# Kernel optimization log

Hardware: AMD Instinct MI355X
Metric: run time of the kernel (lower is better)

Reference implementation:

```python
import jax, jax.numpy as jnp
import numpy as np

BATCH = 4096
INPUT = 14271   # genes
HIDDEN = 24     # gene sets
NUM_ENRICH = 2
EPS = 1e-5          # BatchNorm1d default eps
MAXRANK_PARAM = 1000.0

@jax.custom_vjp
def ste(x):
    # straight-through binarization: forward (x > 0), backward hardtanh(grad)
    return (x > 0).astype(x.dtype)

def _ste_fwd(x):
    return ste(x), None

def _ste_bwd(res, g):
    return (jnp.clip(g, -1.0, 1.0),)

ste.defvjp(_ste_fwd, _ste_bwd)

def setup_inputs() -> dict:
    key = jax.random.key(0)
    ks = jax.random.split(key, 7)
    # ranks in [0, 20000) so that the maxrank clamp is actually exercised
    x_rank = jax.random.uniform(ks[0], (BATCH, INPUT), dtype=jnp.float32) * 20000.0
    x_log2 = jax.random.uniform(ks[1], (BATCH, INPUT), dtype=jnp.float32) * 10.0
    B = jax.random.uniform(ks[2], (INPUT, INPUT), dtype=jnp.float32)
    # matches torch init: normal(mean=-0.1, std=0.055)
    weight = jax.random.normal(ks[3], (INPUT, HIDDEN), dtype=jnp.float32) * 0.055 - 0.1
    maxrank_p = jax.random.uniform(ks[4], (1, 1), dtype=jnp.float32)
    out_w = jax.random.normal(ks[5], (1, HIDDEN * NUM_ENRICH), dtype=jnp.float32) * 0.05
    out_b = jnp.zeros((1,), dtype=jnp.float32)
    return {"x_rank": x_rank, "x_log2": x_log2, "B": B,
            "weight": weight, "maxrank_p": maxrank_p,
            "out_w": out_w, "out_b": out_b}

def reference(x_rank, x_log2, B, weight, maxrank_p, out_w, out_b):
    W = ste(weight)                         # [G, H] binary {0,1}
    n = W.sum(0)[None, :]                   # [1, H] genes per set
    maxrank = n.max() + 10.0 + jnp.maximum(maxrank_p, 0.0) * MAXRANK_PARAM  # [1,1]
    xr = jnp.minimum(x_rank, maxrank)       # clamp ranks
    R = xr @ W                              # [B, H]
    R_UCell = 1.0 - (R - n * (n + 1.0) / 2.0) / (n * maxrank)
    gs_backgrounds = B @ W                  # [G, H]
    bg_score = (x_log2 @ gs_backgrounds) / gs_backgrounds.sum(0)  # [B, H]
    raw_score = (x_log2 @ W) / W.sum(0)     # [B, H]
    R_AMS = raw_score - bg_score
    R_all = jnp.concatenate([R_UCell, R_AMS], axis=1)   # [B, 2H]
    # BatchNorm1d(affine=False), training-mode batch statistics (biased var)
    mu = R_all.mean(0)
    var = R_all.var(0)
    R_norm = (R_all - mu) * jax.lax.rsqrt(var + EPS)
    # dropout treated as identity (eval mode) for deterministic reference
    pred = R_norm @ out_w.T + out_b         # [B, 1]
    return pred
```

## Files before the change

kernel.cpp:

```cpp
#include <hip/hip_runtime.h>
#include <hip/hip_bf16.h>

#define BATCH 4096
#define G     14271
#define H     24
#define KT    446
#define NIT   223
#define MB1   223
#define MBX   64
#define S1    8
#define SX    16
#define IPS1  28
#define IPSX  14
#define GP    14272
#define LDSTR 68
#define FMAX  3.402823466e38f

typedef __bf16 bf16x8 __attribute__((ext_vector_type(8)));
typedef float  f32x4  __attribute__((ext_vector_type(4)));

__device__ inline unsigned short bf16_bits(float f) {
    __bf16 h = (__bf16)f;
    return __builtin_bit_cast(unsigned short, h);
}
__device__ inline float bits_to_f32(unsigned short b) {
    return __builtin_bit_cast(float, (unsigned int)b << 16);
}


__global__ void k_counts(const float* __restrict__ w, int* __restrict__ counts) {
    int g = blockIdx.x * blockDim.x + threadIdx.x;
    bool valid = g < G;
    const float* row = w + (long)g * H;
#pragma unroll
    for (int h = 0; h < H; ++h) {
        bool bit = valid && (row[h] > 0.0f);
        unsigned long long ball = __ballot(bit);
        if ((threadIdx.x & 63) == 0) atomicAdd(&counts[h], (int)__popcll(ball));
    }
}

__global__ void k_consts(const int* __restrict__ counts,
                         const float* __restrict__ maxrank_p,
                         float* __restrict__ consts) {
    __shared__ float smr;
    int t = threadIdx.x;
    if (t == 0) {
        int nm = 0;
        for (int h = 0; h < H; ++h) nm = max(nm, counts[h]);
        float mp = maxrank_p[0];
        if (mp < 0.0f) mp = 0.0f;
        smr = (float)nm + 10.0f + mp * 1000.0f;
        consts[24] = smr;
    }
    __syncthreads();
    if (t < H) {
        float n  = (float)counts[t];
        float mr = smr;
        float c1 = n * (n + 1.0f) * 0.5f;
        float c2 = 1.0f / (n * mr);
        consts[t]      = n;
        consts[32 + t] = 1.0f + c1 * c2;
        consts[56 + t] = c2;
        consts[80 + t] = 1.0f / n;
    }
}

__global__ void k_fillfrag(const float* __restrict__ w,
                           unsigned short* __restrict__ W01f,
                           unsigned short* __restrict__ C2f) {
    int id = blockIdx.x * blockDim.x + threadIdx.x;
    const int nW = KT * 2 * 64;
    const int nC = KT * 3 * 64;
    unsigned short* dst;
    int NT, tl;
    if (id < nW)       { dst = W01f; NT = 2; tl = id; }
    else               { tl = id - nW; if (tl >= nC) return; dst = C2f; NT = 3; }
    int lane  = tl & 63;
    int tile  = tl >> 6;
    int ktile = tile / NT;
    int nt    = tile % NT;
    int col   = nt * 16 + (lane & 15);
    int kbase = ktile * 32 + (lane >> 4) * 8;
    if (dst == C2f && col >= 24) return;
    unsigned short v[8];
#pragma unroll
    for (int j = 0; j < 8; ++j) {
        int k = kbase + j;
        v[j] = (k < G && col < H && (w[(long)k * H + col] > 0.0f))
                   ? (unsigned short)0x3F80 : (unsigned short)0;
    }
    unsigned short* p = dst + ((long)tile * 64 + lane) * 8;
#pragma unroll
    for (int j = 0; j < 8; ++j) p[j] = v[j];
}


__device__ inline void stage_tile(const float* __restrict__ A, int M, int row0,
                                  int k0, bool clampk, float* buf,
                                  int wave, int lane) {
    int k = k0 + lane;
    if (clampk) k = (k < G) ? k : (G - 1);
#pragma unroll
    for (int i = 0; i < 16; ++i) {
        int r = wave * 16 + i;
        int grow = row0 + r;
        grow = (grow < M) ? grow : (M - 1);
        const float* src = A + (long)grow * G + k;
        __builtin_amdgcn_global_load_lds(
            (const __attribute__((address_space(1))) void*)src,
            (__attribute__((address_space(3))) void*)(buf + r * LDSTR),
            4, 0, 0);
    }
}

template <int NT>
__device__ inline void consume_tiles(const float* __restrict__ buf,
                                     const unsigned short* __restrict__ Wf,
                                     int ktile0, float mr, f32x4* acc,
                                     int wave, int lane) {
    int r = lane & 15, sub = lane >> 4;
    const float* rowp = buf + (wave * 16 + r) * LDSTR + sub * 8;
#pragma unroll
    for (int kt = 0; kt < 2; ++kt) {
        const float4* p = reinterpret_cast<const float4*>(rowp + kt * 32);
        float4 lo = p[0];
        float4 hi = p[1];
        float a[8] = {lo.x, lo.y, lo.z, lo.w, hi.x, hi.y, hi.z, hi.w};
        bf16x8 af;
#pragma unroll
        for (int j = 0; j < 8; ++j) af[j] = (__bf16)fminf(a[j], mr);
        const unsigned short* fb = Wf + ((long)((ktile0 + kt) * NT) * 64 + lane) * 8;
#pragma unroll
        for (int nt = 0; nt < NT; ++nt) {
            bf16x8 bfr = *reinterpret_cast<const bf16x8*>(fb + (long)nt * 512);
            acc[nt] = __builtin_amdgcn_mfma_f32_16x16x32_bf16(af, bfr, acc[nt], 0, 0, 0);
        }
    }
}

template <int NT>
__device__ inline void gemm_block(const float* __restrict__ A, int M, int mblk,
                                  const unsigned short* __restrict__ Wf, float mr,
                                  int it0, int it1,
                                  float* __restrict__ outp, int ldo) {
    __shared__ __align__(16) float sbuf[2][64 * LDSTR];
    int wave = threadIdx.x >> 6, lane = threadIdx.x & 63;
    int row0 = mblk * 64;
    f32x4 acc[NT];
#pragma unroll
    for (int nt = 0; nt < NT; ++nt) acc[nt] = (f32x4){0.f, 0.f, 0.f, 0.f};

    stage_tile(A, M, row0, it0 * 64, it0 == NIT - 1, sbuf[0], wave, lane);
    __syncthreads();
    int cur = 0;
    for (int it = it0; it < it1; ++it) {
        if (it + 1 < it1)
            stage_tile(A, M, row0, (it + 1) * 64, (it + 1) == NIT - 1,
                       sbuf[cur ^ 1], wave, lane);
        consume_tiles<NT>(sbuf[cur], Wf, it * 2, mr, acc, wave, lane);
        __syncthreads();
        cur ^= 1;
    }
    int ocol  = lane & 15;
    int sub   = lane >> 4;
    int orow0 = row0 + wave * 16 + sub * 4;
#pragma unroll
    for (int nt = 0; nt < NT; ++nt)
#pragma unroll
        for (int rr = 0; rr < 4; ++rr) {
            int orow = orow0 + rr;
            if (orow < M) outp[(long)orow * ldo + nt * 16 + ocol] = acc[nt][rr];
        }
}

__global__ __launch_bounds__(256) void k_gemm2(
    const float* __restrict__ Bmat, const float* __restrict__ xrank,
    const unsigned short* __restrict__ W01f, const float* __restrict__ consts,
    float* __restrict__ p1, float* __restrict__ rp) {
    int bid = blockIdx.x;
    if (bid < MB1 * S1) {
        int mblk = bid >> 3, split = bid & 7;
        int it0 = split * IPS1;
        int it1 = min(it0 + IPS1, NIT);
        gemm_block<2>(Bmat, G, mblk, W01f, FMAX, it0, it1,
                      p1 + (long)split * GP * 32, 32);
    } else {
        int t = bid - MB1 * S1;
        int mblk = t >> 4, split = t & 15;
        int it0 = split * IPSX;
        int it1 = min(it0 + IPSX, NIT);
        gemm_block<2>(xrank, BATCH, mblk, W01f, consts[24], it0, it1,
                      rp + (long)split * BATCH * 32, 32);
    }
}

__global__ __launch_bounds__(256) void k_gemm3(
    const float* __restrict__ xlog2, const unsigned short* __restrict__ C2f,
    float* __restrict__ lp) {
    int bid = blockIdx.x;
    int mblk = bid >> 4, split = bid & 15;
    int it0 = split * IPSX;
    int it1 = min(it0 + IPSX, NIT);
    gemm_block<3>(xlog2, BATCH, mblk, C2f, FMAX, it0, it1,
                  lp + (long)split * BATCH * 48, 48);
}

__global__ __launch_bounds__(256) void k_reduce1(const float* __restrict__ p1,
                                                 unsigned short* __restrict__ C2f,
                                                 float* __restrict__ blockS) {
    int k = blockIdx.x * 256 + threadIdx.x;
    float gsr[H];
#pragma unroll
    for (int h = 0; h < H; ++h) gsr[h] = 0.0f;
    if (k < GP) {
        if (k < G) {
            for (int sp = 0; sp < S1; ++sp) {
                const float4* r4 = reinterpret_cast<const float4*>(
                    p1 + ((long)sp * GP + k) * 32);
#pragma unroll
                for (int q = 0; q < 6; ++q) {
                    float4 v = r4[q];
                    gsr[q * 4 + 0] += v.x;
                    gsr[q * 4 + 1] += v.y;
                    gsr[q * 4 + 2] += v.z;
                    gsr[q * 4 + 3] += v.w;
                }
            }
        }
        int ktile = k >> 5, j = k & 7, lsub = (k >> 3) & 3;
#pragma unroll
        for (int h = 0; h < H; ++h) {
            unsigned short bits = bf16_bits(gsr[h]);
            int col = 24 + h, nt = col >> 4, lane = lsub * 16 + (col & 15);
            C2f[((long)(ktile * 3 + nt) * 64 + lane) * 8 + j] = bits;
            gsr[h] = bits_to_f32(bits);
        }
    }
    __shared__ float sred[4][H];
    int lane = threadIdx.x & 63, w = threadIdx.x >> 6;
#pragma unroll
    for (int h = 0; h < H; ++h) {
        float v = gsr[h];
        for (int off = 1; off < 64; off <<= 1) v += __shfl_xor(v, off);
        if (lane == 0) sred[w][h] = v;
    }
    __syncthreads();
    if (threadIdx.x < H) {
        float s = sred[0][threadIdx.x] + sred[1][threadIdx.x] +
                  sred[2][threadIdx.x] + sred[3][threadIdx.x];
        blockS[blockIdx.x * H + threadIdx.x] = s;
    }
}

__global__ void k_sumS(const float* __restrict__ blockS, float* __restrict__ consts) {
    int t = threadIdx.x;
    if (t < H) {
        float s = 0.0f;
        for (int b = 0; b < 56; ++b) s += blockS[b * H + t];
        consts[104 + t] = s;
    }
}

__global__ __launch_bounds__(256) void k3a(const float* __restrict__ rp,
                                           const float* __restrict__ lp,
                                           const float* __restrict__ consts,
                                           float* __restrict__ R_all) {
    int e = blockIdx.x * 256 + threadIdx.x;
    if (e >= BATCH * 48) return;
    int b = e / 48, c = e % 48;
    float v;
    if (c < 24) {
        float s = 0.0f;
        for (int sp = 0; sp < SX; ++sp) s += rp[((long)sp * BATCH + b) * 32 + c];
        v = consts[32 + c] - s * consts[56 + c];
    } else {
        int h = c - 24;
        float raw = 0.0f, bg = 0.0f;
        for (int sp = 0; sp < SX; ++sp) {
            const float* base = lp + ((long)sp * BATCH + b) * 48;
            raw += base[h];
            bg  += base[24 + h];
        }
        v = raw * consts[80 + h] - bg / consts[104 + h];
    }
    R_all[e] = v;
}

__global__ __launch_bounds__(256) void k3b(const float* __restrict__ R_all,
                                           const float* __restrict__ out_w,
                                           float* __restrict__ consts) {
    int c = blockIdx.x;
    double s = 0.0, s2 = 0.0;
    for (int b = threadIdx.x; b < BATCH; b += 256) {
        double x = (double)R_all[(long)b * 48 + c];
        s += x; s2 += x * x;
    }
    __shared__ double sh1[256], sh2[256];
    sh1[threadIdx.x] = s; sh2[threadIdx.x] = s2;
    __syncthreads();
    for (int off = 128; off > 0; off >>= 1) {
        if (threadIdx.x < off) {
            sh1[threadIdx.x] += sh1[threadIdx.x + off];
            sh2[threadIdx.x] += sh2[threadIdx.x + off];
        }
        __syncthreads();
    }
    if (threadIdx.x == 0) {
        double mu  = sh1[0] / (double)BATCH;
        double var = sh2[0] / (double)BATCH - mu * mu;
        float rs = (float)(1.0 / sqrt(var + 1e-5));
        consts[128 + c] = (float)mu;
        consts[176 + c] = out_w[c] * rs;
    }
}

__global__ void k3c(const float* __restrict__ R_all, const float* __restrict__ consts,
                    const float* __restrict__ out_b, float* __restrict__ out) {
    int b = blockIdx.x * blockDim.x + threadIdx.x;
    if (b < BATCH) {
        float acc = out_b[0];
#pragma unroll
        for (int c = 0; c < 48; ++c)
            acc += consts[176 + c] * (R_all[(long)b * 48 + c] - consts[128 + c]);
        out[b] = acc;
    }
}


extern "C" void kernel_launch(void* const* d_in, const int* in_sizes, int n_in,
                              void* d_out, int out_size, void* d_ws, size_t ws_size,
                              hipStream_t stream) {
    const float* x_rank    = (const float*)d_in[0];
    const float* x_log2    = (const float*)d_in[1];
    const float* Bmat      = (const float*)d_in[2];
    const float* weight    = (const float*)d_in[3];
    const float* maxrank_p = (const float*)d_in[4];
    const float* out_w     = (const float*)d_in[5];
    const float* out_b     = (const float*)d_in[6];

    char* ws = (char*)d_ws;
    size_t off = 0;
    auto alloc = [&](size_t bytes) {
        void* p = (void*)(ws + off);
        off = (off + bytes + 255) & ~(size_t)255;
        return p;
    };
    float*          consts = (float*)alloc(256 * 4);
    int*            counts = (int*)alloc(128);
    float*          blockS = (float*)alloc(56 * H * 4);
    unsigned short* W01f   = (unsigned short*)alloc((size_t)KT * 2 * 64 * 8 * 2);
    unsigned short* C2f    = (unsigned short*)alloc((size_t)KT * 3 * 64 * 8 * 2);
    float*          p1     = (float*)alloc((size_t)S1 * GP * 32 * 4);
    float*          rp     = (float*)alloc((size_t)SX * BATCH * 32 * 4);
    float*          lp     = (float*)alloc((size_t)SX * BATCH * 48 * 4);
    float*          R_all  = (float*)alloc((size_t)BATCH * 48 * 4);
    (void)ws_size; (void)in_sizes; (void)n_in; (void)out_size;

    hipMemsetAsync(counts, 0, 128, stream);
    k_counts  <<<56, 256, 0, stream>>>(weight, counts);
    k_consts  <<<1, 64, 0, stream>>>(counts, maxrank_p, consts);
    k_fillfrag<<<(KT * 2 * 64 + KT * 3 * 64 + 255) / 256, 256, 0, stream>>>(weight, W01f, C2f);
    k_gemm2   <<<MB1 * S1 + MBX * SX, 256, 0, stream>>>(Bmat, x_rank, W01f, consts, p1, rp);
    k_reduce1 <<<56, 256, 0, stream>>>(p1, C2f, blockS);
    k_sumS    <<<1, 64, 0, stream>>>(blockS, consts);
    k_gemm3   <<<MBX * SX, 256, 0, stream>>>(x_log2, C2f, lp);
    k3a       <<<BATCH * 48 / 256, 256, 0, stream>>>(rp, lp, consts, R_all);
    k3b       <<<48, 256, 0, stream>>>(R_all, out_w, consts);
    k3c       <<<16, 256, 0, stream>>>(R_all, consts, out_b, (float*)d_out);
}
```

Baseline: 381.5 us.

## Use 16-byte swizzled global-to-LDS loads and drop per-iteration block barriers

Staging of A tiles into LDS now issues 16-byte global_load_lds transfers with an XOR swizzle in place of the padded 4-byte-per-lane layout, and the consumer reads use the matching swizzle. This cuts the number of load instructions. Each wave stages and consumes only its own 16 rows, so the __syncthreads per iteration are replaced by s_waitcnt vmcnt plus a sched barrier. The last iteration is peeled off, and launch bounds now request 5 blocks per CU. The risk is correctness if the alignment of row starts (G is odd) breaks the 16-byte assumption or if the vmcnt counts are wrong.

```diff
diff --git a/kernel.cpp b/kernel.cpp
--- a/kernel.cpp
+++ b/kernel.cpp
@@ -13,7 +13,7 @@
 #define IPS1  28
 #define IPSX  14
 #define GP    14272
-#define LDSTR 68
+#define LDW   64
 #define FMAX  3.402823466e38f
 
 typedef __bf16 bf16x8 __attribute__((ext_vector_type(8)));
@@ -96,21 +96,36 @@
 }
 
 
-__device__ inline void stage_tile(const float* __restrict__ A, int M, int row0,
-                                  int k0, bool clampk, float* buf,
-                                  int wave, int lane) {
-    int k = k0 + lane;
-    if (clampk) k = (k < G) ? k : (G - 1);
+
+__device__ inline void stage_tile16(const float* __restrict__ A, int M, int row0,
+                                    int k0, float* buf, int wave, int lane) {
+    int lrb = wave * 16;
+#pragma unroll
+    for (int m = 0; m < 4; ++m) {
+        int lr   = lrb + m * 4 + (lane >> 4);
+        int grow = row0 + lr; grow = (grow < M) ? grow : (M - 1);
+        int lch  = (lane & 15) ^ (lr & 15);
+        const float* src = A + (long)grow * G + k0 + (lch << 2);
+        __builtin_amdgcn_global_load_lds(
+            (const __attribute__((address_space(1))) void*)src,
+            (__attribute__((address_space(3))) void*)(buf + (lrb + m * 4) * LDW),
+            16, 0, 2 );
+    }
+}
+
+__device__ inline void stage_tail4(const float* __restrict__ A, int M, int row0,
+                                   int k0, float* buf, int wave, int lane) {
 #pragma unroll
     for (int i = 0; i < 16; ++i) {
-        int r = wave * 16 + i;
-        int grow = row0 + r;
-        grow = (grow < M) ? grow : (M - 1);
+        int lr   = wave * 16 + i;
+        int grow = row0 + lr; grow = (grow < M) ? grow : (M - 1);
+        int lcol = lane ^ ((lr & 15) << 2);
+        int k    = k0 + lcol; k = (k < G) ? k : (G - 1);
         const float* src = A + (long)grow * G + k;
         __builtin_amdgcn_global_load_lds(
             (const __attribute__((address_space(1))) void*)src,
-            (__attribute__((address_space(3))) void*)(buf + r * LDSTR),
-            4, 0, 0);
+            (__attribute__((address_space(3))) void*)(buf + lr * LDW),
+            4, 0, 2 );
     }
 }
 
@@ -120,12 +135,13 @@
                                      int ktile0, float mr, f32x4* acc,
                                      int wave, int lane) {
     int r = lane & 15, sub = lane >> 4;
-    const float* rowp = buf + (wave * 16 + r) * LDSTR + sub * 8;
+    const float* rowp = buf + (wave * 16 + r) * LDW;
 #pragma unroll
     for (int kt = 0; kt < 2; ++kt) {
-        const float4* p = reinterpret_cast<const float4*>(rowp + kt * 32);
-        float4 lo = p[0];
-        float4 hi = p[1];
+        int c0 = (kt * 8 + 2 * sub + 0) ^ r;
+        int c1 = (kt * 8 + 2 * sub + 1) ^ r;
+        float4 lo = *reinterpret_cast<const float4*>(rowp + (c0 << 2));
+        float4 hi = *reinterpret_cast<const float4*>(rowp + (c1 << 2));
         float a[8] = {lo.x, lo.y, lo.z, lo.w, hi.x, hi.y, hi.z, hi.w};
         bf16x8 af;
 #pragma unroll
@@ -144,24 +160,30 @@
                                   const unsigned short* __restrict__ Wf, float mr,
                                   int it0, int it1,
                                   float* __restrict__ outp, int ldo) {
-    __shared__ __align__(16) float sbuf[2][64 * LDSTR];
+    __shared__ __align__(16) float sbuf[2][64 * LDW];
     int wave = threadIdx.x >> 6, lane = threadIdx.x & 63;
     int row0 = mblk * 64;
     f32x4 acc[NT];
 #pragma unroll
     for (int nt = 0; nt < NT; ++nt) acc[nt] = (f32x4){0.f, 0.f, 0.f, 0.f};
 
-    stage_tile(A, M, row0, it0 * 64, it0 == NIT - 1, sbuf[0], wave, lane);
-    __syncthreads();
+    stage_tile16(A, M, row0, it0 * 64, sbuf[0], wave, lane);
     int cur = 0;
-    for (int it = it0; it < it1; ++it) {
-        if (it + 1 < it1)
-            stage_tile(A, M, row0, (it + 1) * 64, (it + 1) == NIT - 1,
-                       sbuf[cur ^ 1], wave, lane);
+    for (int it = it0; it < it1 - 1; ++it) {
+        int nxt = it + 1;
+        if (nxt == NIT - 1)
+            stage_tail4(A, M, row0, nxt * 64, sbuf[cur ^ 1], wave, lane);
+        else
+            stage_tile16(A, M, row0, nxt * 64, sbuf[cur ^ 1], wave, lane);
+        asm volatile("s_waitcnt vmcnt(4)" ::: "memory");
+        __builtin_amdgcn_sched_barrier(0);
         consume_tiles<NT>(sbuf[cur], Wf, it * 2, mr, acc, wave, lane);
-        __syncthreads();
         cur ^= 1;
     }
+    asm volatile("s_waitcnt vmcnt(0)" ::: "memory");
+    __builtin_amdgcn_sched_barrier(0);
+    consume_tiles<NT>(sbuf[cur], Wf, (it1 - 1) * 2, mr, acc, wave, lane);
+
     int ocol  = lane & 15;
     int sub   = lane >> 4;
     int orow0 = row0 + wave * 16 + sub * 4;
@@ -174,7 +196,7 @@
         }
 }
 
-__global__ __launch_bounds__(256) void k_gemm2(
+__global__ __launch_bounds__(256, 5) void k_gemm2(
     const float* __restrict__ Bmat, const float* __restrict__ xrank,
     const unsigned short* __restrict__ W01f, const float* __restrict__ consts,
     float* __restrict__ p1, float* __restrict__ rp) {
@@ -195,7 +217,7 @@
     }
 }
 
-__global__ __launch_bounds__(256) void k_gemm3(
+__global__ __launch_bounds__(256, 5) void k_gemm3(
     const float* __restrict__ xlog2, const unsigned short* __restrict__ C2f,
     float* __restrict__ lp) {
     int bid = blockIdx.x;
```

Result: slower. 431.9 us (+13.2%).

## Drop split-K for the background GEMM and fuse its reduction into the epilogue

Applied to the files above, without the earlier changes.

The B@W GEMM now runs each 64-row block over the full K range instead of splitting K eight ways. Its epilogue writes the bf16 gene-set backgrounds straight into the C2 fragment buffer and emits per-block column sums. This removes the p1 partial buffer and the separate k_reduce1 kernel. Weight binarization, fragment filling and counting are also merged into one LDS-staged kernel. The cost is far fewer, much longer blocks for the largest GEMM (223 blocks of 223 K-iterations), which may leave the GPU under-occupied and memory-latency bound.

```diff
diff --git a/kernel.cpp b/kernel.cpp
--- a/kernel.cpp
+++ b/kernel.cpp
@@ -8,16 +8,15 @@
 #define NIT   223
 #define MB1   223
 #define MBX   64
-#define S1    8
 #define SX    16
-#define IPS1  28
 #define IPSX  14
-#define GP    14272
 #define LDSTR 68
 #define FMAX  3.402823466e38f
 
 typedef __bf16 bf16x8 __attribute__((ext_vector_type(8)));
 typedef float  f32x4  __attribute__((ext_vector_type(4)));
+typedef unsigned short u16x8 __attribute__((ext_vector_type(8)));
+typedef unsigned short u16x4 __attribute__((ext_vector_type(4)));
 
 __device__ inline unsigned short bf16_bits(float f) {
     __bf16 h = (__bf16)f;
@@ -27,16 +26,64 @@
     return __builtin_bit_cast(float, (unsigned int)b << 16);
 }
 
-
-__global__ void k_counts(const float* __restrict__ w, int* __restrict__ counts) {
-    int g = blockIdx.x * blockDim.x + threadIdx.x;
-    bool valid = g < G;
-    const float* row = w + (long)g * H;
-#pragma unroll
-    for (int h = 0; h < H; ++h) {
-        bool bit = valid && (row[h] > 0.0f);
-        unsigned long long ball = __ballot(bit);
-        if ((threadIdx.x & 63) == 0) atomicAdd(&counts[h], (int)__popcll(ball));
+__global__ __launch_bounds__(256) void k_fillcnt(const float* __restrict__ w,
+                                                 unsigned short* __restrict__ W01f,
+                                                 unsigned short* __restrict__ C2f,
+                                                 int* __restrict__ counts) {
+    __shared__ float wt[4][32 * 24];
+    int wave = threadIdx.x >> 6, lane = threadIdx.x & 63;
+    int wid0 = blockIdx.x * 4 + wave;
+#pragma unroll
+    for (int half = 0; half < 2; ++half) {
+        int kt = wid0 + half * 224;
+        if (kt >= KT) break;
+        {
+            int rloc = lane >> 1;
+            int grow = kt * 32 + rloc;
+            int grc  = (grow < G) ? grow : (G - 1);
+            int col0 = (lane & 1) * 12;
+            const float4* src = reinterpret_cast<const float4*>(w + (long)grc * 24 + col0);
+            float* dst = &wt[wave][rloc * 24 + col0];
+#pragma unroll
+            for (int q = 0; q < 3; ++q) {
+                float4 v = src[q];
+                dst[q * 4 + 0] = v.x; dst[q * 4 + 1] = v.y;
+                dst[q * 4 + 2] = v.z; dst[q * 4 + 3] = v.w;
+            }
+        }
+        int r16 = lane & 15, kloc = (lane >> 4) * 8;
+#pragma unroll
+        for (int nt = 0; nt < 2; ++nt) {
+            int col = nt * 16 + r16;
+            u16x8 v;
+#pragma unroll
+            for (int j = 0; j < 8; ++j) {
+                int k = kt * 32 + kloc + j;
+                bool bit = (k < G) && (col < 24) && (wt[wave][(kloc + j) * 24 + col] > 0.0f);
+                v[j] = bit ? (unsigned short)0x3F80 : (unsigned short)0;
+            }
+            *reinterpret_cast<u16x8*>(W01f + ((long)(kt * 2 + nt) * 64 + lane) * 8) = v;
+        }
+#pragma unroll
+        for (int nt = 0; nt < 2; ++nt) {
+            int col = nt * 16 + r16;
+            if (col >= 24) continue;
+            u16x8 v;
+#pragma unroll
+            for (int j = 0; j < 8; ++j) {
+                int k = kt * 32 + kloc + j;
+                bool bit = (k < G) && (wt[wave][(kloc + j) * 24 + col] > 0.0f);
+                v[j] = bit ? (unsigned short)0x3F80 : (unsigned short)0;
+            }
+            *reinterpret_cast<u16x8*>(C2f + ((long)(kt * 3 + nt) * 64 + lane) * 8) = v;
+        }
+        if (lane < 24) {
+            int c = 0;
+#pragma unroll
+            for (int r = 0; r < 32; ++r)
+                c += ((kt * 32 + r) < G && wt[wave][r * 24 + lane] > 0.0f) ? 1 : 0;
+            atomicAdd(&counts[lane], c);
+        }
     }
 }
 
@@ -66,35 +113,6 @@
     }
 }
 
-__global__ void k_fillfrag(const float* __restrict__ w,
-                           unsigned short* __restrict__ W01f,
-                           unsigned short* __restrict__ C2f) {
-    int id = blockIdx.x * blockDim.x + threadIdx.x;
-    const int nW = KT * 2 * 64;
-    const int nC = KT * 3 * 64;
-    unsigned short* dst;
-    int NT, tl;
-    if (id < nW)       { dst = W01f; NT = 2; tl = id; }
-    else               { tl = id - nW; if (tl >= nC) return; dst = C2f; NT = 3; }
-    int lane  = tl & 63;
-    int tile  = tl >> 6;
-    int ktile = tile / NT;
-    int nt    = tile % NT;
-    int col   = nt * 16 + (lane & 15);
-    int kbase = ktile * 32 + (lane >> 4) * 8;
-    if (dst == C2f && col >= 24) return;
-    unsigned short v[8];
-#pragma unroll
-    for (int j = 0; j < 8; ++j) {
-        int k = kbase + j;
-        v[j] = (k < G && col < H && (w[(long)k * H + col] > 0.0f))
-                   ? (unsigned short)0x3F80 : (unsigned short)0;
-    }
-    unsigned short* p = dst + ((long)tile * 64 + lane) * 8;
-#pragma unroll
-    for (int j = 0; j < 8; ++j) p[j] = v[j];
-}
-
 
 __device__ inline void stage_tile(const float* __restrict__ A, int M, int row0,
                                   int k0, bool clampk, float* buf,
@@ -140,17 +158,13 @@
 }
 
 template <int NT>
-__device__ inline void gemm_block(const float* __restrict__ A, int M, int mblk,
-                                  const unsigned short* __restrict__ Wf, float mr,
-                                  int it0, int it1,
-                                  float* __restrict__ outp, int ldo) {
+__device__ inline void gemm_core(const float* __restrict__ A, int M, int row0,
+                                 const unsigned short* __restrict__ Wf, float mr,
+                                 int it0, int it1, f32x4* acc,
+                                 int wave, int lane) {
     __shared__ __align__(16) float sbuf[2][64 * LDSTR];
-    int wave = threadIdx.x >> 6, lane = threadIdx.x & 63;
-    int row0 = mblk * 64;
-    f32x4 acc[NT];
 #pragma unroll
     for (int nt = 0; nt < NT; ++nt) acc[nt] = (f32x4){0.f, 0.f, 0.f, 0.f};
-
     stage_tile(A, M, row0, it0 * 64, it0 == NIT - 1, sbuf[0], wave, lane);
     __syncthreads();
     int cur = 0;
@@ -162,36 +176,70 @@
         __syncthreads();
         cur ^= 1;
     }
-    int ocol  = lane & 15;
-    int sub   = lane >> 4;
-    int orow0 = row0 + wave * 16 + sub * 4;
-#pragma unroll
-    for (int nt = 0; nt < NT; ++nt)
-#pragma unroll
-        for (int rr = 0; rr < 4; ++rr) {
-            int orow = orow0 + rr;
-            if (orow < M) outp[(long)orow * ldo + nt * 16 + ocol] = acc[nt][rr];
-        }
 }
 
 __global__ __launch_bounds__(256) void k_gemm2(
     const float* __restrict__ Bmat, const float* __restrict__ xrank,
     const unsigned short* __restrict__ W01f, const float* __restrict__ consts,
-    float* __restrict__ p1, float* __restrict__ rp) {
+    unsigned short* __restrict__ C2f, float* __restrict__ blockS,
+    float* __restrict__ rp) {
     int bid = blockIdx.x;
-    if (bid < MB1 * S1) {
-        int mblk = bid >> 3, split = bid & 7;
-        int it0 = split * IPS1;
-        int it1 = min(it0 + IPS1, NIT);
-        gemm_block<2>(Bmat, G, mblk, W01f, FMAX, it0, it1,
-                      p1 + (long)split * GP * 32, 32);
+    int wave = threadIdx.x >> 6, lane = threadIdx.x & 63;
+    int r16 = lane & 15, sub = lane >> 4;
+    f32x4 acc[2];
+    if (bid < MB1) {
+        int mblk = bid, row0 = mblk * 64;
+        gemm_core<2>(Bmat, G, row0, W01f, FMAX, 0, NIT, acc, wave, lane);
+        int gbase = row0 + wave * 16 + sub * 4;
+        int ktile = gbase >> 5;
+        int j0    = gbase & 7;
+        int lsub  = (gbase >> 3) & 3;
+        float colsum[2];
+#pragma unroll
+        for (int nt = 0; nt < 2; ++nt) {
+            u16x4 bits;
+            float cs = 0.0f;
+#pragma unroll
+            for (int rr = 0; rr < 4; ++rr) {
+                int g = gbase + rr;
+                unsigned short b = (g < G) ? bf16_bits(acc[nt][rr]) : (unsigned short)0;
+                bits[rr] = b;
+                cs += bits_to_f32(b);
+            }
+            colsum[nt] = cs;
+            int col = nt * 16 + r16;
+            if (col < 24) {
+                int c = 24 + col;
+                int ntp = c >> 4, lanep = lsub * 16 + (c & 15);
+                *reinterpret_cast<u16x4*>(
+                    C2f + ((long)(ktile * 3 + ntp) * 64 + lanep) * 8 + j0) = bits;
+            }
+        }
+        float v0 = colsum[0], v1 = colsum[1];
+        v0 += __shfl_xor(v0, 16); v0 += __shfl_xor(v0, 32);
+        v1 += __shfl_xor(v1, 16); v1 += __shfl_xor(v1, 32);
+        __shared__ float sred[4][32];
+        if (sub == 0) { sred[wave][r16] = v0; sred[wave][16 + r16] = v1; }
+        __syncthreads();
+        if (threadIdx.x < 24) {
+            int t = threadIdx.x;
+            blockS[mblk * 24 + t] =
+                sred[0][t] + sred[1][t] + sred[2][t] + sred[3][t];
+        }
     } else {
-        int t = bid - MB1 * S1;
+        int t = bid - MB1;
         int mblk = t >> 4, split = t & 15;
         int it0 = split * IPSX;
         int it1 = min(it0 + IPSX, NIT);
-        gemm_block<2>(xrank, BATCH, mblk, W01f, consts[24], it0, it1,
-                      rp + (long)split * BATCH * 32, 32);
+        int row0 = mblk * 64;
+        gemm_core<2>(xrank, BATCH, row0, W01f, consts[24], it0, it1, acc, wave, lane);
+        float* outp = rp + (long)split * BATCH * 32;
+        int orow0 = row0 + wave * 16 + sub * 4;
+#pragma unroll
+        for (int nt = 0; nt < 2; ++nt)
+#pragma unroll
+            for (int rr = 0; rr < 4; ++rr)
+                outp[(long)(orow0 + rr) * 32 + nt * 16 + r16] = acc[nt][rr];
     }
 }
 
@@ -199,65 +247,28 @@
     const float* __restrict__ xlog2, const unsigned short* __restrict__ C2f,
     float* __restrict__ lp) {
     int bid = blockIdx.x;
+    int wave = threadIdx.x >> 6, lane = threadIdx.x & 63;
+    int r16 = lane & 15, sub = lane >> 4;
     int mblk = bid >> 4, split = bid & 15;
     int it0 = split * IPSX;
     int it1 = min(it0 + IPSX, NIT);
-    gemm_block<3>(xlog2, BATCH, mblk, C2f, FMAX, it0, it1,
-                  lp + (long)split * BATCH * 48, 48);
-}
-
-__global__ __launch_bounds__(256) void k_reduce1(const float* __restrict__ p1,
-                                                 unsigned short* __restrict__ C2f,
-                                                 float* __restrict__ blockS) {
-    int k = blockIdx.x * 256 + threadIdx.x;
-    float gsr[H];
-#pragma unroll
-    for (int h = 0; h < H; ++h) gsr[h] = 0.0f;
-    if (k < GP) {
-        if (k < G) {
-            for (int sp = 0; sp < S1; ++sp) {
-                const float4* r4 = reinterpret_cast<const float4*>(
-                    p1 + ((long)sp * GP + k) * 32);
-#pragma unroll
-                for (int q = 0; q < 6; ++q) {
-                    float4 v = r4[q];
-                    gsr[q * 4 + 0] += v.x;
-                    gsr[q * 4 + 1] += v.y;
-                    gsr[q * 4 + 2] += v.z;
-                    gsr[q * 4 + 3] += v.w;
-                }
-            }
-        }
-        int ktile = k >> 5, j = k & 7, lsub = (k >> 3) & 3;
-#pragma unroll
-        for (int h = 0; h < H; ++h) {
-            unsigned short bits = bf16_bits(gsr[h]);
-            int col = 24 + h, nt = col >> 4, lane = lsub * 16 + (col & 15);
-            C2f[((long)(ktile * 3 + nt) * 64 + lane) * 8 + j] = bits;
-            gsr[h] = bits_to_f32(bits);
-        }
-    }
-    __shared__ float sred[4][H];
-    int lane = threadIdx.x & 63, w = threadIdx.x >> 6;
-#pragma unroll
-    for (int h = 0; h < H; ++h) {
-        float v = gsr[h];
-        for (int off = 1; off < 64; off <<= 1) v += __shfl_xor(v, off);
-        if (lane == 0) sred[w][h] = v;
-    }
-    __syncthreads();
-    if (threadIdx.x < H) {
-        float s = sred[0][threadIdx.x] + sred[1][threadIdx.x] +
-                  sred[2][threadIdx.x] + sred[3][threadIdx.x];
-        blockS[blockIdx.x * H + threadIdx.x] = s;
-    }
+    int row0 = mblk * 64;
+    f32x4 acc[3];
+    gemm_core<3>(xlog2, BATCH, row0, C2f, FMAX, it0, it1, acc, wave, lane);
+    float* outp = lp + (long)split * BATCH * 48;
+    int orow0 = row0 + wave * 16 + sub * 4;
+#pragma unroll
+    for (int nt = 0; nt < 3; ++nt)
+#pragma unroll
+        for (int rr = 0; rr < 4; ++rr)
+            outp[(long)(orow0 + rr) * 48 + nt * 16 + r16] = acc[nt][rr];
 }
 
 __global__ void k_sumS(const float* __restrict__ blockS, float* __restrict__ consts) {
     int t = threadIdx.x;
     if (t < H) {
         float s = 0.0f;
-        for (int b = 0; b < 56; ++b) s += blockS[b * H + t];
+        for (int b = 0; b < MB1; ++b) s += blockS[b * 24 + t];
         consts[104 + t] = s;
     }
 }
@@ -348,23 +359,21 @@
     };
     float*          consts = (float*)alloc(256 * 4);
     int*            counts = (int*)alloc(128);
-    float*          blockS = (float*)alloc(56 * H * 4);
+    float*          blockS = (float*)alloc((size_t)MB1 * 24 * 4);
     unsigned short* W01f   = (unsigned short*)alloc((size_t)KT * 2 * 64 * 8 * 2);
     unsigned short* C2f    = (unsigned short*)alloc((size_t)KT * 3 * 64 * 8 * 2);
-    float*          p1     = (float*)alloc((size_t)S1 * GP * 32 * 4);
     float*          rp     = (float*)alloc((size_t)SX * BATCH * 32 * 4);
     float*          lp     = (float*)alloc((size_t)SX * BATCH * 48 * 4);
     float*          R_all  = (float*)alloc((size_t)BATCH * 48 * 4);
     (void)ws_size; (void)in_sizes; (void)n_in; (void)out_size;
 
     hipMemsetAsync(counts, 0, 128, stream);
-    k_counts  <<<56, 256, 0, stream>>>(weight, counts);
+    k_fillcnt <<<56, 256, 0, stream>>>(weight, W01f, C2f, counts);
     k_consts  <<<1, 64, 0, stream>>>(counts, maxrank_p, consts);
-    k_fillfrag<<<(KT * 2 * 64 + KT * 3 * 64 + 255) / 256, 256, 0, stream>>>(weight, W01f, C2f);
-    k_gemm2   <<<MB1 * S1 + MBX * SX, 256, 0, stream>>>(Bmat, x_rank, W01f, consts, p1, rp);
-    k_reduce1 <<<56, 256, 0, stream>>>(p1, C2f, blockS);
+    k_gemm2   <<<MB1 + MBX * SX, 256, 0, stream>>>(Bmat, x_rank, W01f, consts,
+                                                   C2f, blockS, rp);
+    k_gemm3   <<<MBX * SX, 256, 0, stream>>>(x_log2, C2f, lp);
     k_sumS    <<<1, 64, 0, stream>>>(blockS, consts);
-    k_gemm3   <<<MBX * SX, 256, 0, stream>>>(x_log2, C2f, lp);
     k3a       <<<BATCH * 48 / 256, 256, 0, stream>>>(rp, lp, consts, R_all);
     k3b       <<<48, 256, 0, stream>>>(R_all, out_w, consts);
     k3c       <<<16, 256, 0, stream>>>(R_all, consts, out_b, (float*)d_out);
```

New measurement: 634.5 us. 66.3% more time.
